# Optimization experiments

Hardware: AMD Instinct MI355X
Metric: run time of the kernel (lower is better)

The kernel has to match this reference:

```python
import jax, jax.numpy as jnp
from jax import lax
import numpy as np

STRIDES = [4, 8, 16, 32, 64]
SIZES = [32, 64, 128, 256, 512]
RATIOS = [0.5, 1.0, 2.0]
PRE_NMS = 1000   # test-mode pre_nms_topk per level
POST_NMS = 1000  # test-mode post_nms_topk
NMS_THRESH = 0.7
NEG = -1e9
SCALE_CLAMP = float(np.log(1000.0 / 16.0))


def _anchor_bases(size):
    # one size, 3 aspect ratios (h/w); detectron2-style bases centered at 0
    area = float(size) * float(size)
    rows = []
    for ar in RATIOS:
        w = np.sqrt(area / ar)
        h = ar * w
        rows.append([-w / 2.0, -h / 2.0, w / 2.0, h / 2.0])
    return jnp.asarray(np.array(rows, dtype=np.float32))  # [3,4]


def _level_anchors(H, W, stride, bases):
    sx = jnp.arange(W, dtype=jnp.float32) * stride
    sy = jnp.arange(H, dtype=jnp.float32) * stride
    yy, xx = jnp.meshgrid(sy, sx, indexing='ij')
    shifts = jnp.stack([xx, yy, xx, yy], axis=-1).reshape(-1, 1, 4)  # [H*W,1,4]
    return (shifts + bases[None, :, :]).reshape(-1, 4)  # [H*W*3,4]


def _conv(x, w, b, pad):
    y = lax.conv_general_dilated(x, w, (1, 1), [(pad, pad), (pad, pad)],
                                 dimension_numbers=('NCHW', 'OIHW', 'NCHW'))
    return y + b[None, :, None, None]


def _decode(anchors, deltas):
    # anchors [R,4], deltas [B,R,4] -> boxes [B,R,4] (x1,y1,x2,y2)
    w = anchors[:, 2] - anchors[:, 0]
    h = anchors[:, 3] - anchors[:, 1]
    cx = anchors[:, 0] + 0.5 * w
    cy = anchors[:, 1] + 0.5 * h
    dx, dy = deltas[..., 0], deltas[..., 1]
    dw = jnp.minimum(deltas[..., 2], SCALE_CLAMP)
    dh = jnp.minimum(deltas[..., 3], SCALE_CLAMP)
    px = dx * w + cx
    py = dy * h + cy
    pw = jnp.exp(dw) * w
    ph = jnp.exp(dh) * h
    return jnp.stack([px - 0.5 * pw, py - 0.5 * ph, px + 0.5 * pw, py + 0.5 * ph], axis=-1)


def _pairwise_iou(b):
    x1 = jnp.maximum(b[:, None, 0], b[None, :, 0])
    y1 = jnp.maximum(b[:, None, 1], b[None, :, 1])
    x2 = jnp.minimum(b[:, None, 2], b[None, :, 2])
    y2 = jnp.minimum(b[:, None, 3], b[None, :, 3])
    inter = jnp.clip(x2 - x1, 0.0) * jnp.clip(y2 - y1, 0.0)
    area = (b[:, 2] - b[:, 0]) * (b[:, 3] - b[:, 1])
    return inter / (area[:, None] + area[None, :] - inter + 1e-9)


def _nms_single(boxes, scores, valid, lvls, img):
    # greedy batched NMS: level offsets keep levels from suppressing each other
    order = jnp.argsort(-scores)
    b = boxes[order]
    s = scores[order]
    v = valid[order]
    lv = lvls[order].astype(boxes.dtype)
    bo = b + lv[:, None] * (img + 1.0)
    iou = lax.stop_gradient(_pairwise_iou(bo))  # selection is non-differentiable
    T = b.shape[0]
    idxs = jnp.arange(T)

    def step(keep, i):
        supp = (iou[i] > NMS_THRESH) & (idxs > i) & keep[i]
        return keep & ~supp, None

    keep, _ = lax.scan(step, v, jnp.arange(T))
    final = jnp.where(keep, s, NEG)
    topv, topi = lax.top_k(final, POST_NMS)
    return b[topi], topv


def _rpn_forward(feats, w_inter, b_inter, w_logits, b_logits, w_reg, b_reg, image_size):
    img = float(image_size)
    cand_boxes, cand_scores, lvl_ids = [], [], []
    for l, (x, stride, size) in enumerate(zip(feats, STRIDES, SIZES)):
        B, _, H, W = x.shape
        inter = jax.nn.relu(_conv(x, w_inter, b_inter, 1))
        logit = _conv(inter, w_logits, b_logits, 0)        # [B,3,H,W]
        reg = _conv(inter, w_reg, b_reg, 0)                # [B,12,H,W]
        scores = logit.transpose(0, 2, 3, 1).reshape(B, -1)              # [B,H*W*3]
        deltas = reg.reshape(B, 3, 4, H, W).transpose(0, 3, 4, 1, 2).reshape(B, -1, 4)
        anchors = _level_anchors(H, W, stride, _anchor_bases(size))
        boxes = _decode(anchors, deltas)                                  # [B,R,4]
        k = min(PRE_NMS, scores.shape[1])
        topv, topi = lax.top_k(scores, k)
        cand_boxes.append(jnp.take_along_axis(boxes, topi[..., None], axis=1))
        cand_scores.append(topv)
        lvl_ids.append(jnp.full((k,), l, dtype=jnp.int32))
    boxes = jnp.concatenate(cand_boxes, axis=1)   # [B,T,4]
    scores = jnp.concatenate(cand_scores, axis=1) # [B,T]
    lvls = jnp.concatenate(lvl_ids, axis=0)       # [T]
    boxes = jnp.clip(boxes, 0.0, img)
    valid = (boxes[..., 2] > boxes[..., 0]) & (boxes[..., 3] > boxes[..., 1])
    kb, ks = jax.vmap(lambda b, s, v: _nms_single(b, s, v, lvls, img))(boxes, scores, valid)
    return jnp.concatenate([kb, ks[..., None]], axis=-1)  # [B,POST_NMS,5]


def setup_inputs() -> dict:
    key = jax.random.key(0)
    ks = jax.random.split(key, 16)
    C = 256
    inp = {
        'feat_p2': jax.random.normal(ks[0], (2, C, 256, 256), jnp.float32),
        'feat_p3': jax.random.normal(ks[1], (2, C, 128, 128), jnp.float32),
        'feat_p4': jax.random.normal(ks[2], (2, C, 64, 64), jnp.float32),
        'feat_p5': jax.random.normal(ks[3], (2, C, 32, 32), jnp.float32),
        'feat_p6': jax.random.normal(ks[4], (2, C, 16, 16), jnp.float32),
        'w_inter': jax.random.normal(ks[5], (C, C, 3, 3), jnp.float32) * 0.01,
        'b_inter': jnp.zeros((C,), jnp.float32),
        'w_logits': jax.random.normal(ks[6], (3, C, 1, 1), jnp.float32) * 0.01,
        'b_logits': jnp.zeros((3,), jnp.float32),
        'w_reg': jax.random.normal(ks[7], (12, C, 1, 1), jnp.float32) * 0.01,
        'b_reg': jnp.zeros((12,), jnp.float32),
        'image_size': 1024,
    }
    return inp


def reference(feat_p2, feat_p3, feat_p4, feat_p5, feat_p6,
              w_inter, b_inter, w_logits, b_logits, w_reg, b_reg, image_size):
    feats = [feat_p2, feat_p3, feat_p4, feat_p5, feat_p6]
    return _rpn_forward(feats, w_inter, b_inter, w_logits, b_logits, w_reg, b_reg, image_size)
```

## Files before the change

kernel.cpp:

```cpp
#include <hip/hip_runtime.h>
#include <cmath>

typedef unsigned int u32;
typedef unsigned long long u64;

#define TCAND 4768
#define RTOT  261888
#define NW    75
#define NROWS 4800
#define NEGV  -1e9f

__device__ __forceinline__ u32 fkey(float s){
  u32 u = __float_as_uint(s);
  return u ^ ((u >> 31) ? 0xFFFFFFFFu : 0x80000000u);
}

__device__ __forceinline__ void gload_lds16(const float* g, float* l){
  __builtin_amdgcn_global_load_lds((const __attribute__((address_space(1))) void*)g,
                                   (__attribute__((address_space(3))) void*)l, 16, 0, 0);
}
__device__ __forceinline__ void gload_lds4(const float* g, float* l){
  __builtin_amdgcn_global_load_lds((const __attribute__((address_space(1))) void*)g,
                                   (__attribute__((address_space(3))) void*)l, 4, 0, 0);
}

__device__ void bitonic_desc(u64* a, int N, int t, int nt){
  for (int len = 2; len <= N; len <<= 1){
    for (int inc = len >> 1; inc > 0; inc >>= 1){
      __syncthreads();
      for (int idx = t; idx < (N >> 1); idx += nt){
        int i = 2*idx - (idx & (inc - 1));
        int j = i + inc;
        u64 x = a[i], y = a[j];
        bool descR = ((i & len) == 0);
        bool sw = descR ? (x < y) : (x > y);
        if (sw){ a[i] = y; a[j] = x; }
      }
    }
  }
  __syncthreads();
}

__global__ void wtrans(const float* __restrict__ w, float* __restrict__ w_r2,
                       float* __restrict__ zbuf){
  if (blockIdx.x == 0 && threadIdx.x < 16) zbuf[threadIdx.x] = 0.f;
  int idx = blockIdx.x * 256 + threadIdx.x;
  if (idx >= 589824) return;
  int ic = idx / 2304;
  int f  = idx - ic * 2304;
  int tap = f >> 8;
  int oc  = f & 255;
  w_r2[idx] = w[oc * 2304 + ic * 9 + tap];
}

template<int H, int STRIDEV, int ASIZE, int FOFF>
__device__ __forceinline__ void conv_level(
    int rel, const float* __restrict__ feat, const float* __restrict__ w_r2,
    const float* __restrict__ zbuf,
    const float* __restrict__ b_inter, const float* __restrict__ w_logits,
    const float* __restrict__ b_logits, const float* __restrict__ w_reg,
    const float* __restrict__ b_reg, const int* __restrict__ imgp,
    float* __restrict__ score_base, float* __restrict__ box_base,
    float* lds_w, float* lds_x, float* sbuf)
{
  constexpr int W = H;
  constexpr int TX = H / 8;
  constexpr int TILES = TX * TX;
  const int t = threadIdx.x;
  const int img = rel / TILES;
  const int tile = rel - img * TILES;
  const int x0 = (tile % TX) << 3;
  const int y0 = (tile / TX) << 3;
  const int lane = t & 63;
  const int ocg = lane;
  const int r = t >> 6;
  const int q = r;

  const size_t fb = (size_t)img * 256 * H * W;
  const size_t plane = (size_t)H * W;

  const float* xsrc = zbuf;
  size_t xstep = 0;
  if (q == 1 || q == 2){
    int cell = (q - 1) * 64 + lane;
    int xr = cell / 12, xc = cell - xr * 12;
    int gy = y0 + xr - 1, gx = x0 + xc - 1;
    bool ok = (cell < 120) && (xc < 10) && gy >= 0 && gy < H && gx >= 0 && gx < W;
    if (ok){ xsrc = feat + fb + (size_t)gy * W + gx; xstep = plane; }
  }

  float acc[32];
  #pragma unroll
  for (int j = 0; j < 32; j++) acc[j] = 0.f;

  #define STAGE(icv, sb) do { \
    const float* wg_ = w_r2 + (size_t)(icv) * 2304; \
    float* wl_ = lds_w + (sb) * 2304; \
    gload_lds16(wg_ + q * 256 + lane * 4, wl_ + q * 256); \
    if (q == 0) gload_lds16(wg_ + 2048 + lane * 4, wl_ + 2048); \
    if (q == 1 || q == 2) gload_lds4(xsrc + (size_t)(icv) * xstep, \
                                     lds_x + (sb) * 128 + (q - 1) * 64); \
  } while (0)

  STAGE(0, 0);
  STAGE(1, 1);

  int cur = 0;
  #pragma unroll 1
  for (int ic = 0; ic < 256; ++ic){
    __builtin_amdgcn_s_barrier();
    __builtin_amdgcn_sched_barrier(0);
    if (ic < 254){
      int sb = cur + 2; if (sb >= 3) sb -= 3;
      STAGE(ic + 2, sb);
    }
    __builtin_amdgcn_sched_barrier(0);
    if (ic < 254){
      if (q < 3) asm volatile("s_waitcnt vmcnt(4)" ::: "memory");
      else       asm volatile("s_waitcnt vmcnt(2)" ::: "memory");
    } else if (ic == 254){
      if (q < 3) asm volatile("s_waitcnt vmcnt(2)" ::: "memory");
      else       asm volatile("s_waitcnt vmcnt(1)" ::: "memory");
    } else {
      asm volatile("s_waitcnt vmcnt(0)" ::: "memory");
    }
    __builtin_amdgcn_sched_barrier(0);
    __builtin_amdgcn_s_barrier();
    __builtin_amdgcn_sched_barrier(0);

    const float* wbuf = lds_w + cur * 2304;
    const float* xbuf = lds_x + cur * 128;
    #pragma unroll
    for (int ky = 0; ky < 3; ky++){
      float xrow[10];
      {
        const float* xp = xbuf + (r + ky) * 12;
        *(float4*)&xrow[0] = *(const float4*)xp;
        *(float4*)&xrow[4] = *(const float4*)(xp + 4);
        *(float2*)&xrow[8] = *(const float2*)(xp + 8);
      }
      #pragma unroll
      for (int kx = 0; kx < 3; kx++){
        const int tap = ky * 3 + kx;
        float wk[4];
        *(float4*)&wk[0] = *(const float4*)(wbuf + tap * 256 + ocg * 4);
        #pragma unroll
        for (int k = 0; k < 4; k++){
          #pragma unroll
          for (int c = 0; c < 8; c++)
            acc[k * 8 + c] = __builtin_fmaf(wk[k], xrow[c + kx], acc[k * 8 + c]);
        }
      }
    }
    cur = cur + 1; if (cur == 3) cur = 0;
  }
  #undef STAGE

  {
    float bb[4];
    *(float4*)&bb[0] = *(const float4*)(b_inter + ocg * 4);
    #pragma unroll
    for (int k = 0; k < 4; k++)
      #pragma unroll
      for (int c = 0; c < 8; c++)
        acc[k * 8 + c] = fmaxf(acc[k * 8 + c] + bb[k], 0.f);
  }

  const int grp = ocg & 60;
  #pragma unroll 1
  for (int o = 0; o < 15; o++){
    const float* whp = (o < 3) ? (w_logits + o * 256) : (w_reg + (o - 3) * 256);
    float wh4[4];
    *(float4*)&wh4[0] = *(const float4*)(whp + ocg * 4);
    float fin[8];
    #pragma unroll
    for (int c = 0; c < 8; c++){
      float t1 = 0.f;
      #pragma unroll
      for (int k = 0; k < 4; k++) t1 = __builtin_fmaf(wh4[k], acc[k * 8 + c], t1);
      float b1 = __shfl(t1, grp);
      float t2 = b1;
      #pragma unroll
      for (int k = 0; k < 4; k++) t2 = __builtin_fmaf(wh4[k], acc[k * 8 + c], t2);
      float b2 = __shfl(t2, grp + 1);
      float t3 = b2;
      #pragma unroll
      for (int k = 0; k < 4; k++) t3 = __builtin_fmaf(wh4[k], acc[k * 8 + c], t3);
      float b3 = __shfl(t3, grp + 2);
      float t4 = b3;
      #pragma unroll
      for (int k = 0; k < 4; k++) t4 = __builtin_fmaf(wh4[k], acc[k * 8 + c], t4);
      float v = t4 + __shfl_xor(t4, 4);
      v = v + __shfl_xor(v, 8);
      v = v + __shfl_xor(v, 16);
      v = v + __shfl_xor(v, 32);
      fin[c] = v;
    }
    if (ocg == 3){
      #pragma unroll
      for (int c = 0; c < 8; c++) sbuf[(r * 8 + c) * 16 + o] = fin[c];
    }
  }
  __syncthreads();

  if (t < 192){
    int a = t >> 6; int px = t & 63;
    int rr = px >> 3, cc = px & 7;
    int y = y0 + rr, x = x0 + cc;
    float img_f = (float)(*imgp);
    float sc = sbuf[px * 16 + a] + b_logits[a];
    float d0 = sbuf[px * 16 + 3 + a * 4 + 0] + b_reg[a * 4 + 0];
    float d1 = sbuf[px * 16 + 3 + a * 4 + 1] + b_reg[a * 4 + 1];
    float d2 = sbuf[px * 16 + 3 + a * 4 + 2] + b_reg[a * 4 + 2];
    float d3 = sbuf[px * 16 + 3 + a * 4 + 3] + b_reg[a * 4 + 3];
    double ar = (a == 0) ? 0.5 : ((a == 1) ? 1.0 : 2.0);
    double area_d = (double)ASIZE * (double)ASIZE;
    double wd = sqrt(area_d / ar);
    double hd = ar * wd;
    float bx1 = (float)(-wd * 0.5), by1 = (float)(-hd * 0.5);
    float bx2 = (float)( wd * 0.5), by2 = (float)( hd * 0.5);
    float sx = (float)(x * STRIDEV), sy = (float)(y * STRIDEV);
    float ax1 = sx + bx1, ay1 = sy + by1, ax2 = sx + bx2, ay2 = sy + by2;
    float aw = __fsub_rn(ax2, ax1), ah = __fsub_rn(ay2, ay1);
    float acx = __fadd_rn(ax1, __fmul_rn(0.5f, aw));
    float acy = __fadd_rn(ay1, __fmul_rn(0.5f, ah));
    const float CLAMP = (float)4.135166556742356;
    float dwv = fminf(d2, CLAMP), dhv = fminf(d3, CLAMP);
    float pcx = __fadd_rn(__fmul_rn(d0, aw), acx);
    float pcy = __fadd_rn(__fmul_rn(d1, ah), acy);
    float pw = __fmul_rn((float)exp((double)dwv), aw);
    float ph = __fmul_rn((float)exp((double)dhv), ah);
    float hx = __fmul_rn(0.5f, pw), hy = __fmul_rn(0.5f, ph);
    float X1 = __fsub_rn(pcx, hx), Y1 = __fsub_rn(pcy, hy);
    float X2 = __fadd_rn(pcx, hx), Y2 = __fadd_rn(pcy, hy);
    X1 = fminf(fmaxf(X1, 0.f), img_f); Y1 = fminf(fmaxf(Y1, 0.f), img_f);
    X2 = fminf(fmaxf(X2, 0.f), img_f); Y2 = fminf(fmaxf(Y2, 0.f), img_f);
    int gi = (y * W + x) * 3 + a;
    size_t oidx = (size_t)img * RTOT + FOFF + gi;
    score_base[oidx] = sc;
    ((float4*)box_base)[oidx] = make_float4(X1, Y1, X2, Y2);
  }
}

__global__ __launch_bounds__(512, 4) void conv_all(
    const float* __restrict__ f2, const float* __restrict__ f3,
    const float* __restrict__ f4, const float* __restrict__ f5,
    const float* __restrict__ f6, const float* __restrict__ w_r2,
    const float* __restrict__ zbuf,
    const float* __restrict__ b_inter, const float* __restrict__ w_logits,
    const float* __restrict__ b_logits, const float* __restrict__ w_reg,
    const float* __restrict__ b_reg, const int* __restrict__ imgp,
    float* __restrict__ score_base, float* __restrict__ box_base)
{
  __shared__ float lds_w[3 * 2304];
  __shared__ float lds_x[3 * 128];
  __shared__ float sbuf[64 * 16];
  const int bid = blockIdx.x;
  if (bid < 2048)
    conv_level<256, 4, 32, 0>(bid, f2, w_r2, zbuf, b_inter, w_logits, b_logits, w_reg,
                              b_reg, imgp, score_base, box_base, lds_w, lds_x, sbuf);
  else if (bid < 2560)
    conv_level<128, 8, 64, 196608>(bid - 2048, f3, w_r2, zbuf, b_inter, w_logits, b_logits,
                                   w_reg, b_reg, imgp, score_base, box_base, lds_w, lds_x, sbuf);
  else if (bid < 2688)
    conv_level<64, 16, 128, 245760>(bid - 2560, f4, w_r2, zbuf, b_inter, w_logits, b_logits,
                                    w_reg, b_reg, imgp, score_base, box_base, lds_w, lds_x, sbuf);
  else if (bid < 2720)
    conv_level<32, 32, 256, 258048>(bid - 2688, f5, w_r2, zbuf, b_inter, w_logits, b_logits,
                                    w_reg, b_reg, imgp, score_base, box_base, lds_w, lds_x, sbuf);
  else
    conv_level<16, 64, 512, 261120>(bid - 2720, f6, w_r2, zbuf, b_inter, w_logits, b_logits,
                                    w_reg, b_reg, imgp, score_base, box_base, lds_w, lds_x, sbuf);
}

__global__ __launch_bounds__(1024) void topk_lvl(
    const float* __restrict__ score_base, const float* __restrict__ box_base,
    float* __restrict__ cs, float* __restrict__ cb, int* __restrict__ clvl)
{
  const int lvl = blockIdx.x, b = blockIdx.y;
  const int Rtab[5] = {196608, 49152, 12288, 3072, 768};
  const int Ktab[5] = {1000, 1000, 1000, 1000, 768};
  const int Ftab[5] = {0, 196608, 245760, 258048, 261120};
  const int Ctab[5] = {0, 1000, 2000, 3000, 4000};
  const int R = Rtab[lvl], kk = Ktab[lvl], foff = Ftab[lvl], coff = Ctab[lvl];
  const float* sc = score_base + (size_t)b * RTOT + foff;
  const int t = threadIdx.x;
  __shared__ u32 hist[256];
  __shared__ u32 sh_prefix, sh_r;
  __shared__ u32 cgt, ceq;
  __shared__ u64 sel[1024];
  __shared__ u64 eqb[1024];
  if (t == 0){ sh_prefix = 0u; sh_r = (u32)kk; }
  __syncthreads();
  for (int pass = 0; pass < 4; ++pass){
    if (t < 256) hist[t] = 0u;
    __syncthreads();
    u32 prefix = sh_prefix;
    int shift = 24 - 8 * pass;
    u32 maskHi = (pass == 0) ? 0u : (0xFFFFFFFFu << (shift + 8));
    for (int i = t; i < R; i += 1024){
      u32 key = fkey(sc[i]);
      if ((key & maskHi) == prefix) atomicAdd(&hist[(key >> shift) & 255u], 1u);
    }
    __syncthreads();
    if (t == 0){
      u32 r = sh_r; u32 run = 0; int chosen = 255;
      for (int bv = 255; bv >= 0; --bv){
        u32 c = hist[bv];
        if (run + c >= r){ chosen = bv; break; }
        run += c;
      }
      sh_prefix = prefix | ((u32)chosen << shift);
      sh_r = r - run;
    }
    __syncthreads();
  }
  const u32 Tkey = sh_prefix; const u32 need_eq = sh_r;
  if (t == 0){ cgt = 0u; ceq = 0u; }
  __syncthreads();
  for (int i = t; i < R; i += 1024){
    u32 key = fkey(sc[i]);
    if (key > Tkey){
      u32 p = atomicAdd(&cgt, 1u);
      sel[p] = (((u64)key) << 32) | (u64)(0xFFFFFFFFu - (u32)i);
    } else if (key == Tkey){
      u32 e = atomicAdd(&ceq, 1u);
      if (e < 1024u) eqb[e] = (u64)(0xFFFFFFFFu - (u32)i);
    }
  }
  __syncthreads();
  u32 nGt = cgt; u32 nEq = ceq > 1024u ? 1024u : ceq;
  if ((u32)t >= nEq) eqb[t] = 0ull;
  __syncthreads();
  bitonic_desc(eqb, 1024, t, 1024);
  if ((u32)t < need_eq) sel[nGt + t] = (((u64)Tkey) << 32) | (eqb[t] & 0xFFFFFFFFull);
  if (t >= kk) sel[t] = 0ull;
  __syncthreads();
  bitonic_desc(sel, 1024, t, 1024);
  if (t < kk){
    u64 v = sel[t];
    u32 i = 0xFFFFFFFFu - (u32)(v & 0xFFFFFFFFull);
    int dst = b * TCAND + coff + t;
    cs[dst] = sc[i];
    ((float4*)cb)[dst] = ((const float4*)box_base)[(size_t)b * RTOT + foff + i];
    clvl[dst] = lvl;
  }
}

__global__ __launch_bounds__(1024) void gsort(
    const float* __restrict__ cs, const float* __restrict__ cb, const int* __restrict__ clvl,
    const int* __restrict__ imgp,
    float* __restrict__ s_score, float* __restrict__ s_box, float* __restrict__ obox,
    float* __restrict__ area, int* __restrict__ validarr)
{
  const int b = blockIdx.x, t = threadIdx.x;
  __shared__ u64 arr[8192];
  for (int i = t; i < 8192; i += 1024){
    u64 v = 0ull;
    if (i < TCAND){
      u32 key = fkey(cs[b * TCAND + i]);
      v = (((u64)key) << 32) | (u64)(0xFFFFFFFFu - (u32)i);
    }
    arr[i] = v;
  }
  __syncthreads();
  bitonic_desc(arr, 8192, t, 1024);
  const float img = (float)(*imgp);
  const float off1 = img + 1.0f;
  for (int s = t; s < TCAND; s += 1024){
    u32 ci = 0xFFFFFFFFu - (u32)(arr[s] & 0xFFFFFFFFull);
    int src = b * TCAND + (int)ci;
    int dst = b * TCAND + s;
    float scv = cs[src];
    float4 bx = ((const float4*)cb)[src];
    s_score[dst] = scv;
    ((float4*)s_box)[dst] = bx;
    float lv = (float)clvl[src];
    float tt = __fmul_rn(lv, off1);
    float o0 = __fadd_rn(bx.x, tt), o1 = __fadd_rn(bx.y, tt);
    float o2 = __fadd_rn(bx.z, tt), o3 = __fadd_rn(bx.w, tt);
    ((float4*)obox)[dst] = make_float4(o0, o1, o2, o3);
    area[dst] = __fmul_rn(__fsub_rn(o2, o0), __fsub_rn(o3, o1));
    validarr[dst] = (bx.z > bx.x && bx.w > bx.y) ? 1 : 0;
  }
}

__global__ void iou_mat(const float* __restrict__ obox, const float* __restrict__ area,
                        u64* __restrict__ supp)
{
  const int b = blockIdx.y;
  int wid = blockIdx.x * 256 + threadIdx.x;
  const int total = TCAND * NW;
  if (wid >= total) return;
  int i = wid / NW, w = wid - i * NW;
  float4 bi = ((const float4*)obox)[b * TCAND + i];
  float ai = area[b * TCAND + i];
  u64 bits = 0ull;
  int jbase = w << 6;
  for (int jj = 0; jj < 64; jj++){
    int j = jbase + jj;
    if (j >= TCAND) break;
    if (j <= i) continue;
    float4 bj = ((const float4*)obox)[b * TCAND + j];
    float xx1 = fmaxf(bi.x, bj.x), yy1 = fmaxf(bi.y, bj.y);
    float xx2 = fminf(bi.z, bj.z), yy2 = fminf(bi.w, bj.w);
    float iw = fmaxf(__fsub_rn(xx2, xx1), 0.f);
    float ih = fmaxf(__fsub_rn(yy2, yy1), 0.f);
    float inter = __fmul_rn(iw, ih);
    float uni = __fadd_rn(__fsub_rn(__fadd_rn(ai, area[b * TCAND + j]), inter), 1e-9f);
    float iou = inter / uni;
    if (iou > 0.7f) bits |= (1ull << jj);
  }
  supp[((size_t)b * NROWS + i) * NW + w] = bits;
}

__global__ __launch_bounds__(64) void nms_scan(const u64* __restrict__ supp,
                                               const int* __restrict__ validarr,
                                               u64* __restrict__ keep_out)
{
  const int b = blockIdx.x;
  const int lane = threadIdx.x;
  u64 rlo = 0ull, rhi = 0ull;
  for (int jj = 0; jj < 64; jj++){
    int i1 = (lane << 6) + jj;
    u64 bad1 = (i1 < TCAND) ? (validarr[b * TCAND + i1] ? 0ull : 1ull) : 1ull;
    rlo |= bad1 << jj;
    int i2 = ((lane + 64) << 6) + jj;
    u64 bad2 = (i2 < TCAND) ? (validarr[b * TCAND + i2] ? 0ull : 1ull) : 1ull;
    rhi |= bad2 << jj;
  }
  for (int c = 0; c < NW; c++){
    u64 rw = (c < 64) ? __shfl(rlo, c) : __shfl(rhi, c - 64);
    u64 diag = supp[((size_t)b * NROWS + (c << 6) + lane) * NW + c];
    for (int s = 0; s < 64; s++){
      if (!((rw >> s) & 1ull)) rw |= __shfl(diag, s);
    }
    if (c < 64){ if (lane == c) rlo = rw; }
    else       { if (lane == c - 64) rhi = rw; }
    u64 kept = ~rw;
    const u64* rowbase = supp + ((size_t)b * NROWS + (c << 6)) * NW;
    for (int s = 0; s < 64; s++){
      if ((kept >> s) & 1ull){
        rlo |= rowbase[(size_t)s * NW + lane];
        if (lane < 11) rhi |= rowbase[(size_t)s * NW + 64 + lane];
      }
    }
  }
  keep_out[b * 80 + lane] = ~rlo;
  if (lane < 11) keep_out[b * 80 + 64 + lane] = ~rhi;
}

__global__ __launch_bounds__(1024) void emit(const u64* __restrict__ keep_out,
                                             const float* __restrict__ s_score,
                                             const float* __restrict__ s_box,
                                             float* __restrict__ out)
{
  const int b = blockIdx.x, t = threadIdx.x;
  __shared__ int part[1024];
  int f[5]; int base = t * 5; int lsum = 0;
  #pragma unroll
  for (int q = 0; q < 5; q++){
    int s = base + q; int kp = 0;
    if (s < TCAND) kp = (int)((keep_out[b * 80 + (s >> 6)] >> (s & 63)) & 1ull);
    f[q] = kp; lsum += kp;
  }
  part[t] = lsum;
  __syncthreads();
  for (int d = 1; d < 1024; d <<= 1){
    int addv = 0;
    if (t >= d) addv = part[t - d];
    __syncthreads();
    part[t] += addv;
    __syncthreads();
  }
  int K = part[1023];
  int kcnt = part[t] - lsum;
  #pragma unroll
  for (int q = 0; q < 5; q++){
    int s = base + q;
    if (s < TCAND){
      int pos = f[q] ? kcnt : (K + (s - kcnt));
      if (pos < 1000){
        float4 bx = ((const float4*)s_box)[b * TCAND + s];
        float scv = f[q] ? s_score[b * TCAND + s] : NEGV;
        float* o = out + ((size_t)b * 1000 + pos) * 5;
        o[0] = bx.x; o[1] = bx.y; o[2] = bx.z; o[3] = bx.w; o[4] = scv;
      }
      kcnt += f[q];
    }
  }
}

extern "C" void kernel_launch(void* const* d_in, const int* in_sizes, int n_in,
                              void* d_out, int out_size, void* d_ws, size_t ws_size,
                              hipStream_t stream)
{
  (void)in_sizes; (void)n_in; (void)out_size; (void)ws_size;
  const float* f2 = (const float*)d_in[0];
  const float* f3 = (const float*)d_in[1];
  const float* f4 = (const float*)d_in[2];
  const float* f5 = (const float*)d_in[3];
  const float* f6 = (const float*)d_in[4];
  const float* w_inter  = (const float*)d_in[5];
  const float* b_inter  = (const float*)d_in[6];
  const float* w_logits = (const float*)d_in[7];
  const float* b_logits = (const float*)d_in[8];
  const float* w_reg    = (const float*)d_in[9];
  const float* b_reg    = (const float*)d_in[10];
  const int*   imgp     = (const int*)d_in[11];

  char* ws = (char*)d_ws;
  float* w_r2       = (float*)(ws + 0);
  float* score_base = (float*)(ws + 2359296);
  float* box_base   = (float*)(ws + 4454400);
  float* cs         = (float*)(ws + 12834816);
  float* cb         = (float*)(ws + 12872960);
  int*   clvl       = (int*)  (ws + 13025536);
  float* s_score    = (float*)(ws + 13063680);
  float* s_box      = (float*)(ws + 13101824);
  float* obox       = (float*)(ws + 13254400);
  float* area       = (float*)(ws + 13406976);
  int*   validarr   = (int*)  (ws + 13445120);
  u64*   supp       = (u64*)  (ws + 13483264);
  u64*   keep_out   = (u64*)  (ws + 19243264);
  float* zbuf       = (float*)(ws + 13483264);

  hipLaunchKernelGGL(wtrans, dim3((589824 + 255) / 256), dim3(256), 0, stream,
                     w_inter, w_r2, zbuf);

  hipLaunchKernelGGL(conv_all, dim3(2728), dim3(512), 0, stream,
                     f2, f3, f4, f5, f6, w_r2, zbuf, b_inter, w_logits, b_logits,
                     w_reg, b_reg, imgp, score_base, box_base);

  hipLaunchKernelGGL(topk_lvl, dim3(5, 2), dim3(1024), 0, stream,
                     score_base, box_base, cs, cb, clvl);
  hipLaunchKernelGGL(gsort, dim3(2), dim3(1024), 0, stream,
                     cs, cb, clvl, imgp, s_score, s_box, obox, area, validarr);
  hipLaunchKernelGGL(iou_mat, dim3((TCAND * NW + 255) / 256, 2), dim3(256), 0, stream,
                     obox, area, supp);
  hipLaunchKernelGGL(nms_scan, dim3(2), dim3(64), 0, stream, supp, validarr, keep_out);
  hipLaunchKernelGGL(emit, dim3(2), dim3(1024), 0, stream, keep_out, s_score, s_box,
                     (float*)d_out);
}
```

Measured before the change: 4.752 ms.

## Stage two input channels per barrier with double buffering in conv; branchless NMS row OR

The 3x3 conv main loop now loads weights and inputs for two input channels per stage. It uses double buffering instead of a three-deep single-channel ring, which halves the number of barrier and wait cycles per block. The waitcnt accounting is redone for the new per-wave load counts, and launch bounds are raised to request 5 blocks per CU. LDS use per block grows (about 37KB for weights), which may limit occupancy, and prefetch depth drops to one stage. Separately, the NMS suppression-row accumulation replaces the per-bit conditional load with a masked unconditional load, unrolled by 4.

```diff
diff --git a/kernel.cpp b/kernel.cpp
--- a/kernel.cpp
+++ b/kernel.cpp
@@ -89,38 +89,42 @@
     if (ok){ xsrc = feat + fb + (size_t)gy * W + gx; xstep = plane; }
   }
 
+  const int c0 = 2 * q, c1 = 2 * q + 1;
+  const int cex = (q == 0) ? 16 : ((q == 3) ? 17 : -1);
+
   float acc[32];
   #pragma unroll
   for (int j = 0; j < 32; j++) acc[j] = 0.f;
 
-  #define STAGE(icv, sb) do { \
-    const float* wg_ = w_r2 + (size_t)(icv) * 2304; \
-    float* wl_ = lds_w + (sb) * 2304; \
-    gload_lds16(wg_ + q * 256 + lane * 4, wl_ + q * 256); \
-    if (q == 0) gload_lds16(wg_ + 2048 + lane * 4, wl_ + 2048); \
-    if (q == 1 || q == 2) gload_lds4(xsrc + (size_t)(icv) * xstep, \
-                                     lds_x + (sb) * 128 + (q - 1) * 64); \
+  #define STAGE(g_, sb) do { \
+    const float* wg_ = w_r2 + (size_t)(g_) * 4608; \
+    float* wl_ = lds_w + (sb) * 4608; \
+    gload_lds16(wg_ + c0 * 256 + lane * 4, wl_ + c0 * 256); \
+    gload_lds16(wg_ + c1 * 256 + lane * 4, wl_ + c1 * 256); \
+    if (cex >= 0) gload_lds16(wg_ + cex * 256 + lane * 4, wl_ + cex * 256); \
+    if (q == 1 || q == 2){ \
+      gload_lds4(xsrc + (size_t)(2 * (g_)) * xstep, \
+                 lds_x + (sb) * 256 + (q - 1) * 64); \
+      gload_lds4(xsrc + (size_t)(2 * (g_) + 1) * xstep, \
+                 lds_x + (sb) * 256 + 128 + (q - 1) * 64); \
+    } \
   } while (0)
 
   STAGE(0, 0);
-  STAGE(1, 1);
 
   int cur = 0;
   #pragma unroll 1
-  for (int ic = 0; ic < 256; ++ic){
+  for (int g = 0; g < 128; ++g){
     __builtin_amdgcn_s_barrier();
     __builtin_amdgcn_sched_barrier(0);
-    if (ic < 254){
-      int sb = cur + 2; if (sb >= 3) sb -= 3;
-      STAGE(ic + 2, sb);
+    if (g < 127){
+      STAGE(g + 1, cur ^ 1);
     }
     __builtin_amdgcn_sched_barrier(0);
-    if (ic < 254){
-      if (q < 3) asm volatile("s_waitcnt vmcnt(4)" ::: "memory");
-      else       asm volatile("s_waitcnt vmcnt(2)" ::: "memory");
-    } else if (ic == 254){
-      if (q < 3) asm volatile("s_waitcnt vmcnt(2)" ::: "memory");
-      else       asm volatile("s_waitcnt vmcnt(1)" ::: "memory");
+    if (g < 127){
+      if (q == 1 || q == 2)      asm volatile("s_waitcnt vmcnt(4)" ::: "memory");
+      else if (q == 0 || q == 3) asm volatile("s_waitcnt vmcnt(3)" ::: "memory");
+      else                       asm volatile("s_waitcnt vmcnt(2)" ::: "memory");
     } else {
       asm volatile("s_waitcnt vmcnt(0)" ::: "memory");
     }
@@ -128,31 +132,36 @@
     __builtin_amdgcn_s_barrier();
     __builtin_amdgcn_sched_barrier(0);
 
-    const float* wbuf = lds_w + cur * 2304;
-    const float* xbuf = lds_x + cur * 128;
+    const float* wbuf = lds_w + cur * 4608;
+    const float* xbuf = lds_x + cur * 256;
     #pragma unroll
-    for (int ky = 0; ky < 3; ky++){
-      float xrow[10];
-      {
-        const float* xp = xbuf + (r + ky) * 12;
-        *(float4*)&xrow[0] = *(const float4*)xp;
-        *(float4*)&xrow[4] = *(const float4*)(xp + 4);
-        *(float2*)&xrow[8] = *(const float2*)(xp + 8);
-      }
-      #pragma unroll
-      for (int kx = 0; kx < 3; kx++){
-        const int tap = ky * 3 + kx;
-        float wk[4];
-        *(float4*)&wk[0] = *(const float4*)(wbuf + tap * 256 + ocg * 4);
+    for (int icl = 0; icl < 2; icl++){
+      const float* wsub = wbuf + icl * 2304;
+      const float* xsub = xbuf + icl * 128;
+      #pragma unroll
+      for (int ky = 0; ky < 3; ky++){
+        float xrow[10];
+        {
+          const float* xp = xsub + (r + ky) * 12;
+          *(float4*)&xrow[0] = *(const float4*)xp;
+          *(float4*)&xrow[4] = *(const float4*)(xp + 4);
+          *(float2*)&xrow[8] = *(const float2*)(xp + 8);
+        }
         #pragma unroll
-        for (int k = 0; k < 4; k++){
+        for (int kx = 0; kx < 3; kx++){
+          const int tap = ky * 3 + kx;
+          float wk[4];
+          *(float4*)&wk[0] = *(const float4*)(wsub + tap * 256 + ocg * 4);
           #pragma unroll
-          for (int c = 0; c < 8; c++)
-            acc[k * 8 + c] = __builtin_fmaf(wk[k], xrow[c + kx], acc[k * 8 + c]);
+          for (int k = 0; k < 4; k++){
+            #pragma unroll
+            for (int c = 0; c < 8; c++)
+              acc[k * 8 + c] = __builtin_fmaf(wk[k], xrow[c + kx], acc[k * 8 + c]);
+          }
         }
       }
     }
-    cur = cur + 1; if (cur == 3) cur = 0;
+    cur ^= 1;
   }
   #undef STAGE
 
@@ -242,7 +251,7 @@
   }
 }
 
-__global__ __launch_bounds__(512, 4) void conv_all(
+__global__ __launch_bounds__(512, 5) void conv_all(
     const float* __restrict__ f2, const float* __restrict__ f3,
     const float* __restrict__ f4, const float* __restrict__ f5,
     const float* __restrict__ f6, const float* __restrict__ w_r2,
@@ -252,8 +261,8 @@
     const float* __restrict__ b_reg, const int* __restrict__ imgp,
     float* __restrict__ score_base, float* __restrict__ box_base)
 {
-  __shared__ float lds_w[3 * 2304];
-  __shared__ float lds_x[3 * 128];
+  __shared__ float lds_w[2 * 4608];
+  __shared__ float lds_x[2 * 256];
   __shared__ float sbuf[64 * 16];
   const int bid = blockIdx.x;
   if (bid < 2048)
@@ -439,11 +448,11 @@
     else       { if (lane == c - 64) rhi = rw; }
     u64 kept = ~rw;
     const u64* rowbase = supp + ((size_t)b * NROWS + (c << 6)) * NW;
+    #pragma unroll 4
     for (int s = 0; s < 64; s++){
-      if ((kept >> s) & 1ull){
-        rlo |= rowbase[(size_t)s * NW + lane];
-        if (lane < 11) rhi |= rowbase[(size_t)s * NW + 64 + lane];
-      }
+      u64 m = 0ull - ((kept >> s) & 1ull);
+      rlo |= rowbase[(size_t)s * NW + lane] & m;
+      if (lane < 11) rhi |= rowbase[(size_t)s * NW + 64 + lane] & m;
     }
   }
   keep_out[b * 80 + lane] = ~rlo;
```

Result: slower. 5.819 ms (+22.5%).

## Enlarge conv tile to 16x8 pixels with two rows per wave

Applied to the files above, without the earlier changes.

Each block in the fused 3x3 conv now covers a 16-row by 8-column spatial tile instead of 8x8. Each wave accumulates two output rows (64 accumulators per thread), and four waves stage the larger input halo, so every weight fetched into LDS is reused across twice as many pixels. This halves the block count and the per-pixel cost of staging weights, at the price of higher register pressure under launch bounds of (512,4). The ky loop is no longer unrolled, which may add loop overhead.

```diff
diff --git a/kernel.cpp b/kernel.cpp
--- a/kernel.cpp
+++ b/kernel.cpp
@@ -64,42 +64,43 @@
     float* lds_w, float* lds_x, float* sbuf)
 {
   constexpr int W = H;
-  constexpr int TX = H / 8;
-  constexpr int TILES = TX * TX;
+  constexpr int TXC = W / 8;
+  constexpr int TYR = H / 16;
+  constexpr int TILES = TXC * TYR;
   const int t = threadIdx.x;
   const int img = rel / TILES;
   const int tile = rel - img * TILES;
-  const int x0 = (tile % TX) << 3;
-  const int y0 = (tile / TX) << 3;
+  const int x0 = (tile % TXC) << 3;
+  const int y0 = (tile / TXC) << 4;
   const int lane = t & 63;
   const int ocg = lane;
-  const int r = t >> 6;
-  const int q = r;
+  const int u = t >> 6;
+  const int q = u;
 
   const size_t fb = (size_t)img * 256 * H * W;
   const size_t plane = (size_t)H * W;
 
   const float* xsrc = zbuf;
   size_t xstep = 0;
-  if (q == 1 || q == 2){
+  if (q >= 1 && q <= 4){
     int cell = (q - 1) * 64 + lane;
     int xr = cell / 12, xc = cell - xr * 12;
     int gy = y0 + xr - 1, gx = x0 + xc - 1;
-    bool ok = (cell < 120) && (xc < 10) && gy >= 0 && gy < H && gx >= 0 && gx < W;
+    bool ok = (cell < 216) && (xc < 10) && gy >= 0 && gy < H && gx >= 0 && gx < W;
     if (ok){ xsrc = feat + fb + (size_t)gy * W + gx; xstep = plane; }
   }
 
-  float acc[32];
+  float acc[64];
   #pragma unroll
-  for (int j = 0; j < 32; j++) acc[j] = 0.f;
+  for (int j = 0; j < 64; j++) acc[j] = 0.f;
 
   #define STAGE(icv, sb) do { \
     const float* wg_ = w_r2 + (size_t)(icv) * 2304; \
     float* wl_ = lds_w + (sb) * 2304; \
     gload_lds16(wg_ + q * 256 + lane * 4, wl_ + q * 256); \
     if (q == 0) gload_lds16(wg_ + 2048 + lane * 4, wl_ + 2048); \
-    if (q == 1 || q == 2) gload_lds4(xsrc + (size_t)(icv) * xstep, \
-                                     lds_x + (sb) * 128 + (q - 1) * 64); \
+    if (q >= 1 && q <= 4) gload_lds4(xsrc + (size_t)(icv) * xstep, \
+                                     lds_x + (sb) * 256 + (q - 1) * 64); \
   } while (0)
 
   STAGE(0, 0);
@@ -116,11 +117,11 @@
     }
     __builtin_amdgcn_sched_barrier(0);
     if (ic < 254){
-      if (q < 3) asm volatile("s_waitcnt vmcnt(4)" ::: "memory");
-      else       asm volatile("s_waitcnt vmcnt(2)" ::: "memory");
+      if (q <= 4) asm volatile("s_waitcnt vmcnt(4)" ::: "memory");
+      else        asm volatile("s_waitcnt vmcnt(2)" ::: "memory");
     } else if (ic == 254){
-      if (q < 3) asm volatile("s_waitcnt vmcnt(2)" ::: "memory");
-      else       asm volatile("s_waitcnt vmcnt(1)" ::: "memory");
+      if (q <= 4) asm volatile("s_waitcnt vmcnt(2)" ::: "memory");
+      else        asm volatile("s_waitcnt vmcnt(1)" ::: "memory");
     } else {
       asm volatile("s_waitcnt vmcnt(0)" ::: "memory");
     }
@@ -129,26 +130,31 @@
     __builtin_amdgcn_sched_barrier(0);
 
     const float* wbuf = lds_w + cur * 2304;
-    const float* xbuf = lds_x + cur * 128;
-    #pragma unroll
+    const float* xbuf = lds_x + cur * 256;
+    #pragma unroll 1
     for (int ky = 0; ky < 3; ky++){
-      float xrow[10];
+      float xr0[10], xr1[10];
       {
-        const float* xp = xbuf + (r + ky) * 12;
-        *(float4*)&xrow[0] = *(const float4*)xp;
-        *(float4*)&xrow[4] = *(const float4*)(xp + 4);
-        *(float2*)&xrow[8] = *(const float2*)(xp + 8);
+        const float* xp0 = xbuf + (2 * u + ky) * 12;
+        *(float4*)&xr0[0] = *(const float4*)xp0;
+        *(float4*)&xr0[4] = *(const float4*)(xp0 + 4);
+        *(float2*)&xr0[8] = *(const float2*)(xp0 + 8);
+        const float* xp1 = xp0 + 12;
+        *(float4*)&xr1[0] = *(const float4*)xp1;
+        *(float4*)&xr1[4] = *(const float4*)(xp1 + 4);
+        *(float2*)&xr1[8] = *(const float2*)(xp1 + 8);
       }
       #pragma unroll
       for (int kx = 0; kx < 3; kx++){
-        const int tap = ky * 3 + kx;
         float wk[4];
-        *(float4*)&wk[0] = *(const float4*)(wbuf + tap * 256 + ocg * 4);
+        *(float4*)&wk[0] = *(const float4*)(wbuf + (ky * 3 + kx) * 256 + ocg * 4);
         #pragma unroll
         for (int k = 0; k < 4; k++){
           #pragma unroll
-          for (int c = 0; c < 8; c++)
-            acc[k * 8 + c] = __builtin_fmaf(wk[k], xrow[c + kx], acc[k * 8 + c]);
+          for (int c = 0; c < 16; c++){
+            float xv = (c < 8) ? xr0[(c & 7) + kx] : xr1[(c & 7) + kx];
+            acc[k * 16 + c] = __builtin_fmaf(wk[k], xv, acc[k * 16 + c]);
+          }
         }
       }
     }
@@ -162,8 +168,8 @@
     #pragma unroll
     for (int k = 0; k < 4; k++)
       #pragma unroll
-      for (int c = 0; c < 8; c++)
-        acc[k * 8 + c] = fmaxf(acc[k * 8 + c] + bb[k], 0.f);
+      for (int c = 0; c < 16; c++)
+        acc[k * 16 + c] = fmaxf(acc[k * 16 + c] + bb[k], 0.f);
   }
 
   const int grp = ocg & 60;
@@ -172,39 +178,34 @@
     const float* whp = (o < 3) ? (w_logits + o * 256) : (w_reg + (o - 3) * 256);
     float wh4[4];
     *(float4*)&wh4[0] = *(const float4*)(whp + ocg * 4);
-    float fin[8];
     #pragma unroll
-    for (int c = 0; c < 8; c++){
+    for (int c = 0; c < 16; c++){
       float t1 = 0.f;
       #pragma unroll
-      for (int k = 0; k < 4; k++) t1 = __builtin_fmaf(wh4[k], acc[k * 8 + c], t1);
+      for (int k = 0; k < 4; k++) t1 = __builtin_fmaf(wh4[k], acc[k * 16 + c], t1);
       float b1 = __shfl(t1, grp);
       float t2 = b1;
       #pragma unroll
-      for (int k = 0; k < 4; k++) t2 = __builtin_fmaf(wh4[k], acc[k * 8 + c], t2);
+      for (int k = 0; k < 4; k++) t2 = __builtin_fmaf(wh4[k], acc[k * 16 + c], t2);
       float b2 = __shfl(t2, grp + 1);
       float t3 = b2;
       #pragma unroll
-      for (int k = 0; k < 4; k++) t3 = __builtin_fmaf(wh4[k], acc[k * 8 + c], t3);
+      for (int k = 0; k < 4; k++) t3 = __builtin_fmaf(wh4[k], acc[k * 16 + c], t3);
       float b3 = __shfl(t3, grp + 2);
       float t4 = b3;
       #pragma unroll
-      for (int k = 0; k < 4; k++) t4 = __builtin_fmaf(wh4[k], acc[k * 8 + c], t4);
+      for (int k = 0; k < 4; k++) t4 = __builtin_fmaf(wh4[k], acc[k * 16 + c], t4);
       float v = t4 + __shfl_xor(t4, 4);
       v = v + __shfl_xor(v, 8);
       v = v + __shfl_xor(v, 16);
       v = v + __shfl_xor(v, 32);
-      fin[c] = v;
-    }
-    if (ocg == 3){
-      #pragma unroll
-      for (int c = 0; c < 8; c++) sbuf[(r * 8 + c) * 16 + o] = fin[c];
-    }
-  }
-  __syncthreads();
-
-  if (t < 192){
-    int a = t >> 6; int px = t & 63;
+      if (ocg == 3) sbuf[(u * 16 + c) * 16 + o] = v;
+    }
+  }
+  __syncthreads();
+
+  if (t < 384){
+    int a = t >> 7; int px = t & 127;
     int rr = px >> 3, cc = px & 7;
     int y = y0 + rr, x = x0 + cc;
     float img_f = (float)(*imgp);
@@ -253,23 +254,23 @@
     float* __restrict__ score_base, float* __restrict__ box_base)
 {
   __shared__ float lds_w[3 * 2304];
-  __shared__ float lds_x[3 * 128];
-  __shared__ float sbuf[64 * 16];
+  __shared__ float lds_x[3 * 256];
+  __shared__ float sbuf[128 * 16];
   const int bid = blockIdx.x;
-  if (bid < 2048)
+  if (bid < 1024)
     conv_level<256, 4, 32, 0>(bid, f2, w_r2, zbuf, b_inter, w_logits, b_logits, w_reg,
                               b_reg, imgp, score_base, box_base, lds_w, lds_x, sbuf);
-  else if (bid < 2560)
-    conv_level<128, 8, 64, 196608>(bid - 2048, f3, w_r2, zbuf, b_inter, w_logits, b_logits,
+  else if (bid < 1280)
+    conv_level<128, 8, 64, 196608>(bid - 1024, f3, w_r2, zbuf, b_inter, w_logits, b_logits,
                                    w_reg, b_reg, imgp, score_base, box_base, lds_w, lds_x, sbuf);
-  else if (bid < 2688)
-    conv_level<64, 16, 128, 245760>(bid - 2560, f4, w_r2, zbuf, b_inter, w_logits, b_logits,
+  else if (bid < 1344)
+    conv_level<64, 16, 128, 245760>(bid - 1280, f4, w_r2, zbuf, b_inter, w_logits, b_logits,
                                     w_reg, b_reg, imgp, score_base, box_base, lds_w, lds_x, sbuf);
-  else if (bid < 2720)
-    conv_level<32, 32, 256, 258048>(bid - 2688, f5, w_r2, zbuf, b_inter, w_logits, b_logits,
+  else if (bid < 1360)
+    conv_level<32, 32, 256, 258048>(bid - 1344, f5, w_r2, zbuf, b_inter, w_logits, b_logits,
                                     w_reg, b_reg, imgp, score_base, box_base, lds_w, lds_x, sbuf);
   else
-    conv_level<16, 64, 512, 261120>(bid - 2720, f6, w_r2, zbuf, b_inter, w_logits, b_logits,
+    conv_level<16, 64, 512, 261120>(bid - 1360, f6, w_r2, zbuf, b_inter, w_logits, b_logits,
                                     w_reg, b_reg, imgp, score_base, box_base, lds_w, lds_x, sbuf);
 }
 
@@ -528,7 +529,7 @@
   hipLaunchKernelGGL(wtrans, dim3((589824 + 255) / 256), dim3(256), 0, stream,
                      w_inter, w_r2, zbuf);
 
-  hipLaunchKernelGGL(conv_all, dim3(2728), dim3(512), 0, stream,
+  hipLaunchKernelGGL(conv_all, dim3(1364), dim3(512), 0, stream,
                      f2, f3, f4, f5, f6, w_r2, zbuf, b_inter, w_logits, b_logits,
                      w_reg, b_reg, imgp, score_base, box_base);
 
```

After: 4.996 ms. +5.1%, slower.
